# Kernel optimization log

Hardware: AMD Instinct MI355X
Metric: run time of the kernel (lower is better)

Reference implementation:

```python
import jax, jax.numpy as jnp
import numpy as np

B, L, A, D = 4, 512, 8, 256
H = 256  # hidden_dim
O = 256  # output_dim


def setup_inputs() -> dict:
    key = jax.random.key(0)
    ks = jax.random.split(key, 12)
    s = 0.05
    return {
        "x": jax.random.normal(ks[0], (B, L, A, D), dtype=jnp.float32),
        "conv_w": jax.random.normal(ks[1], (H, D), dtype=jnp.float32) * s,
        "conv_b": jax.random.normal(ks[2], (H,), dtype=jnp.float32) * s,
        "theta_w": jax.random.normal(ks[3], (H, H), dtype=jnp.float32) * s,
        "theta_b": jax.random.normal(ks[4], (H,), dtype=jnp.float32) * s,
        "phi_w": jax.random.normal(ks[5], (H, H), dtype=jnp.float32) * s,
        "phi_b": jax.random.normal(ks[6], (H,), dtype=jnp.float32) * s,
        "g_w": jax.random.normal(ks[7], (H, H), dtype=jnp.float32) * s,
        "g_b": jax.random.normal(ks[8], (H,), dtype=jnp.float32) * s,
        "f_w": jax.random.normal(ks[9], (O, H), dtype=jnp.float32) * s,
        "f_b": jax.random.normal(ks[10], (O,), dtype=jnp.float32) * s,
    }


def reference(x, conv_w, conv_b, theta_w, theta_b, phi_w, phi_b, g_w, g_b, f_w, f_b):
    batch, length, n_agents, _ = x.shape
    # residual: identity (input_dim == output_dim, stride 1)
    res = x
    # conv with kernel (1,1): pointwise projection over channel dim
    h = jnp.einsum('blad,hd->blah', x, conv_w) + conv_b  # [B,L,A,H]
    N = length * n_agents
    h = h.reshape(batch, N, H)
    theta = jnp.einsum('bnh,kh->bnk', h, theta_w) + theta_b  # [B,N,H]
    phi = jnp.einsum('bnh,kh->bnk', h, phi_w) + phi_b        # [B,N,H]
    g = jnp.einsum('bnh,kh->bnk', h, g_w) + g_b              # [B,N,H]
    scores = jnp.einsum('bnk,bmk->bnm', theta, phi) / jnp.sqrt(jnp.asarray(H, theta.dtype))
    y = jax.nn.softmax(scores, axis=2)                       # [B,N,N]
    z = jnp.einsum('bnm,bmk->bnk', y, g) / jnp.sqrt(jnp.asarray(N, y.dtype))
    out = jnp.einsum('bnk,ok->bno', z, f_w) + f_b            # [B,N,O]
    out = out.reshape(batch, length, n_agents, O)
    return out + res
```

## Files before the change

kernel.cpp:

```cpp
#include <hip/hip_runtime.h>

typedef unsigned short u16;
typedef __bf16 bf16x8 __attribute__((ext_vector_type(8)));
typedef float f32x4 __attribute__((ext_vector_type(4)));
typedef float f32x16 __attribute__((ext_vector_type(16)));
typedef float float4v __attribute__((ext_vector_type(4)));
typedef unsigned short u16x8 __attribute__((ext_vector_type(8)));
typedef unsigned short u16x4 __attribute__((ext_vector_type(4)));

#define MFMA16(a, b, c) __builtin_amdgcn_mfma_f32_16x16x32_bf16(a, b, c, 0, 0, 0)
#define MFMA32(a, b, c) __builtin_amdgcn_mfma_f32_32x32x16_bf16(a, b, c, 0, 0, 0)

__device__ __forceinline__ u16 f2bf(float f) {
  union { float f; unsigned u; } v; v.f = f;
  unsigned r = v.u + 0x7fffu + ((v.u >> 16) & 1u);
  return (u16)(r >> 16);
}
__device__ __forceinline__ float bf2f(u16 b) {
  union { unsigned u; float f; } v; v.u = ((unsigned)b) << 16;
  return v.f;
}

__device__ __forceinline__ void gload16(const void* g, void* l) {
  __builtin_amdgcn_global_load_lds(
      (__attribute__((address_space(1))) void*)g,
      (__attribute__((address_space(3))) void*)l, 16, 0, 0);
}

__device__ __forceinline__ unsigned cvtpk(float lo, float hi) {
  unsigned r;
  asm("v_cvt_pk_bf16_f32 %0, %1, %2" : "=v"(r) : "v"(lo), "v"(hi));
  return r;
}
__device__ __forceinline__ void plswap(unsigned& a, unsigned& b) {
  asm volatile("v_permlane32_swap_b32 %0, %1" : "+v"(a), "+v"(b));
}

__global__ __launch_bounds__(256) void convert_w(
    const float* __restrict__ cw,
    const float* __restrict__ tw, const float* __restrict__ pw,
    const float* __restrict__ gw, const float* __restrict__ fw,
    const float* __restrict__ tb, const float* __restrict__ pb,
    const float* __restrict__ gb,
    u16* __restrict__ cwb, u16* __restrict__ wcat, u16* __restrict__ fwb,
    float* __restrict__ bcat) {
  const int idx = blockIdx.x * 256 + threadIdx.x;
  const float* src;
  u16* dst;
  int off;
  if (idx < 16384)      { src = cw; dst = cwb;  off = idx; }
  else if (idx < 32768) { src = tw; dst = wcat; off = idx - 16384; }
  else if (idx < 49152) { src = pw; dst = wcat + 65536;  off = idx - 32768; }
  else if (idx < 65536) { src = gw; dst = wcat + 131072; off = idx - 49152; }
  else if (idx < 81920) { src = fw; dst = fwb;  off = idx - 65536; }
  else if (idx < 82112) {
    int j = (idx - 81920) * 4;
#pragma unroll
    for (int i = 0; i < 4; ++i) {
      int k = j + i;
      bcat[k] = (k < 256) ? tb[k] : (k < 512) ? pb[k - 256] : gb[k - 512];
    }
    return;
  } else return;
  float4v v = *(const float4v*)(src + (size_t)off * 4);
  u16x4 o;
#pragma unroll
  for (int i = 0; i < 4; ++i) o[i] = f2bf(v[i]);
  *(u16x4*)(dst + (size_t)off * 4) = o;
}

__global__ __launch_bounds__(256) void gemm_bt(
    const u16* __restrict__ A, const u16* __restrict__ W,
    const float* __restrict__ bias, u16* __restrict__ Cout, int K, int ldc) {
  __shared__ u16 As[8192];
  __shared__ u16 Bs[8192];
  const int t = threadIdx.x;
  const int lane = t & 63, w = t >> 6;
  const int brow = blockIdx.x * 128, bcol = blockIdx.y * 128;
  const int wr = (w >> 1) * 64, wc = (w & 1) * 64;
  f32x4 acc[4][4];
#pragma unroll
  for (int i = 0; i < 4; ++i)
#pragma unroll
    for (int j = 0; j < 4; ++j)
#pragma unroll
      for (int r = 0; r < 4; ++r) acc[i][j][r] = 0.0f;

  const int sr = t >> 3, sc8 = (t & 7) * 8;
  const u16* gA = A + (size_t)(brow + sr) * K + sc8;
  const u16* gW = W + (size_t)(bcol + sr) * K + sc8;

  for (int kt = 0; kt < K; kt += 64) {
#pragma unroll
    for (int c = 0; c < 4; ++c) {
      gload16(gA + (size_t)c * 32 * K + kt, &As[c * 2048 + t * 8]);
      gload16(gW + (size_t)c * 32 * K + kt, &Bs[c * 2048 + t * 8]);
    }
    __syncthreads();
#pragma unroll
    for (int kk = 0; kk < 2; ++kk) {
      const int ko = kk * 32 + (lane >> 4) * 8;
      bf16x8 af[4], bfr[4];
#pragma unroll
      for (int i = 0; i < 4; ++i)
        af[i] = *(const bf16x8*)(&As[(wr + i * 16 + (lane & 15)) * 64 + ko]);
#pragma unroll
      for (int j = 0; j < 4; ++j)
        bfr[j] = *(const bf16x8*)(&Bs[(wc + j * 16 + (lane & 15)) * 64 + ko]);
#pragma unroll
      for (int i = 0; i < 4; ++i)
#pragma unroll
        for (int j = 0; j < 4; ++j)
          acc[i][j] = MFMA16(af[i], bfr[j], acc[i][j]);
    }
    __syncthreads();
  }

  const int r0 = (lane >> 4) * 4, c0 = lane & 15;
#pragma unroll
  for (int i = 0; i < 4; ++i)
#pragma unroll
    for (int j = 0; j < 4; ++j) {
      const int col = bcol + wc + j * 16 + c0;
      const float bv = bias[col];
#pragma unroll
      for (int r = 0; r < 4; ++r) {
        const size_t o = (size_t)(brow + wr + i * 16 + r0 + r) * ldc + col;
        Cout[o] = f2bf(acc[i][j][r] + bv);
      }
    }
}

__global__ __launch_bounds__(256) void gemm_h(
    const float* __restrict__ X, const u16* __restrict__ W,
    const float* __restrict__ bias, u16* __restrict__ Cout) {
  __shared__ u16 As[8192];
  __shared__ u16 Bs[8192];
  const int t = threadIdx.x;
  const int lane = t & 63, w = t >> 6;
  const int brow = blockIdx.x * 128, bcol = blockIdx.y * 128;
  const int wr = (w >> 1) * 64, wc = (w & 1) * 64;
  f32x4 acc[4][4];
#pragma unroll
  for (int i = 0; i < 4; ++i)
#pragma unroll
    for (int j = 0; j < 4; ++j)
#pragma unroll
      for (int r = 0; r < 4; ++r) acc[i][j][r] = 0.0f;

  const int sr = t >> 3, sc8 = (t & 7) * 8;
  const u16* gW = W + (size_t)(bcol + sr) * 256 + sc8;
  const int ar = t & 127, ach = t >> 7;
  const float* gX = X + (size_t)(brow + ar) * 256 + ach * 32;

  for (int kt = 0; kt < 256; kt += 64) {
#pragma unroll
    for (int c = 0; c < 4; ++c)
      gload16(gW + (size_t)c * 32 * 256 + kt, &Bs[c * 2048 + t * 8]);
    u16x8 pk[4];
#pragma unroll
    for (int j = 0; j < 4; ++j) {
      float4v v0 = *(const float4v*)(gX + kt + j * 8);
      float4v v1 = *(const float4v*)(gX + kt + j * 8 + 4);
#pragma unroll
      for (int e = 0; e < 4; ++e) { pk[j][e] = f2bf(v0[e]); pk[j][4 + e] = f2bf(v1[e]); }
    }
#pragma unroll
    for (int j = 0; j < 4; ++j) {
      int unit = (ach * 4 + j) ^ (ar & 7);
      *(u16x8*)(&As[ar * 64 + unit * 8]) = pk[j];
    }
    __syncthreads();
#pragma unroll
    for (int kk = 0; kk < 2; ++kk) {
      const int ko = kk * 32 + (lane >> 4) * 8;
      bf16x8 af[4], bfr[4];
#pragma unroll
      for (int i = 0; i < 4; ++i) {
        int R = wr + i * 16 + (lane & 15);
        int unit = (kk * 4 + (lane >> 4)) ^ (R & 7);
        af[i] = *(const bf16x8*)(&As[R * 64 + unit * 8]);
      }
#pragma unroll
      for (int j = 0; j < 4; ++j)
        bfr[j] = *(const bf16x8*)(&Bs[(wc + j * 16 + (lane & 15)) * 64 + ko]);
#pragma unroll
      for (int i = 0; i < 4; ++i)
#pragma unroll
        for (int j = 0; j < 4; ++j)
          acc[i][j] = MFMA16(af[i], bfr[j], acc[i][j]);
    }
    __syncthreads();
  }

  const int r0 = (lane >> 4) * 4, c0 = lane & 15;
#pragma unroll
  for (int i = 0; i < 4; ++i)
#pragma unroll
    for (int j = 0; j < 4; ++j) {
      const int col = bcol + wc + j * 16 + c0;
      const float bv = bias[col];
#pragma unroll
      for (int r = 0; r < 4; ++r) {
        const size_t o = (size_t)(brow + wr + i * 16 + r0 + r) * 256 + col;
        Cout[o] = f2bf(acc[i][j][r] + bv);
      }
    }
}

__global__ __launch_bounds__(256) void transpose_g_k(
    const u16* __restrict__ tpg, u16* __restrict__ gT) {
  __shared__ u16 T[64][65];
  const int t = threadIdx.x;
  const int bm = (blockIdx.x & 63) * 64;
  const int bk = ((blockIdx.x >> 6) & 3) * 64;
  const int b = blockIdx.x >> 8;
  const int r = t >> 3, c8 = (t & 7) * 8;
#pragma unroll
  for (int ch = 0; ch < 2; ++ch) {
    u16x8 v = *(const u16x8*)(tpg + (size_t)(b * 4096 + bm + r + ch * 32) * 768 + 512 + bk + c8);
#pragma unroll
    for (int j = 0; j < 8; ++j) T[r + ch * 32][c8 + j] = v[j];
  }
  __syncthreads();
#pragma unroll
  for (int ch = 0; ch < 2; ++ch) {
    u16x8 o;
#pragma unroll
    for (int j = 0; j < 8; ++j) o[j] = T[c8 + j][r + ch * 32];
    *(u16x8*)(gT + (size_t)(b * 256 + bk + r + ch * 32) * 4096 + bm + c8) = o;
  }
}

__global__ __launch_bounds__(256, 2) void flash2(
    const u16* __restrict__ tpg, const u16* __restrict__ gT,
    u16* __restrict__ Zp, u16* __restrict__ Lpb) {
  __shared__ u16 Kl[2][32 * 256];
  __shared__ u16 Vl[2][256 * 32];

  const int t = threadIdx.x;
  const int lane = t & 63, w = t >> 6;
  const int l31 = lane & 31, hi = lane >> 5;
  const int bid = blockIdx.x;
  const int b = bid >> 7;
  const int quarter = (bid >> 5) & 3;
  const int qt = bid & 31;
  const int q0 = qt * 128 + w * 32;
  const int kv0 = quarter * 1024;

  bf16x8 q[16];
  {
    const u16* qp = tpg + (size_t)(b * 4096 + q0 + l31) * 768 + hi * 8;
#pragma unroll
    for (int ks = 0; ks < 16; ++ks) q[ks] = *(const bf16x8*)(qp + ks * 16);
  }

  f32x16 zacc[8];
#pragma unroll
  for (int i = 0; i < 8; ++i)
#pragma unroll
    for (int j = 0; j < 16; ++j) zacc[i][j] = 0.0f;
  float ell = 0.0f;

  const int ksr = t >> 5, ksc = t & 31;

  auto stage = [&](int tile, int bi) {
    const size_t krow0 = (size_t)(b * 4096 + kv0 + tile * 32);
#pragma unroll
    for (int ch = 0; ch < 4; ++ch) {
      int r = ch * 8 + ksr;
      gload16(tpg + (krow0 + r) * 768 + 256 + ((ksc ^ r) * 8), &Kl[bi][ch * 2048 + t * 8]);
    }
#pragma unroll
    for (int ch = 0; ch < 4; ++ch) {
      int u = ch * 256 + t;
      int r = u >> 2, c16 = u & 3;
      gload16(gT + (size_t)(b * 256 + r) * 4096 + kv0 + tile * 32 + ((c16 ^ ((r >> 1) & 3)) * 8),
              &Vl[bi][u * 8]);
    }
  };

  stage(0, 0);
  __syncthreads();

  for (int tile = 0; tile < 32; ++tile) {
    const int cur = tile & 1;
    if (tile + 1 < 32) stage(tile + 1, cur ^ 1);

    f32x16 s;
#pragma unroll
    for (int j = 0; j < 16; ++j) s[j] = 0.0f;
    const u16* kb = &Kl[cur][0];
    __builtin_amdgcn_s_setprio(1);
#pragma unroll
    for (int ks = 0; ks < 16; ++ks) {
      bf16x8 kf = *(const bf16x8*)(kb + l31 * 256 + (((2 * ks + hi) ^ l31) * 8));
      s = MFMA32(kf, q[ks], s);
    }
    __builtin_amdgcn_s_setprio(0);

    bf16x8 pa[2];
#pragma unroll
    for (int half = 0; half < 2; ++half) {
      float p[8];
#pragma unroll
      for (int g = 0; g < 8; ++g) {
        p[g] = __builtin_amdgcn_exp2f(s[half * 8 + g] * 0.09016844f);
        ell += p[g];
      }
      unsigned x0 = cvtpk(p[0], p[1]), y0 = cvtpk(p[4], p[5]);
      unsigned x1 = cvtpk(p[2], p[3]), y1 = cvtpk(p[6], p[7]);
      plswap(x0, y0);
      plswap(x1, y1);
      union { unsigned u[4]; bf16x8 v; } cc;
      cc.u[0] = x0; cc.u[1] = x1; cc.u[2] = y0; cc.u[3] = y1;
      pa[half] = cc.v;
    }

    const u16* vb = &Vl[cur][0];
    __builtin_amdgcn_s_setprio(1);
#pragma unroll
    for (int ks2 = 0; ks2 < 2; ++ks2) {
#pragma unroll
      for (int nt = 0; nt < 8; ++nt) {
        int row = nt * 32 + l31;
        bf16x8 vv = *(const bf16x8*)(vb + row * 32 + (((2 * ks2 + hi) ^ ((row >> 1) & 3)) * 8));
        zacc[nt] = MFMA32(pa[ks2], vv, zacc[nt]);
      }
    }
    __builtin_amdgcn_s_setprio(0);
    __syncthreads();
  }

  ell += __shfl_xor(ell, 32, 64);

#pragma unroll
  for (int g = 0; g < 16; ++g) {
    int r = (g & 3) + 8 * (g >> 2) + 4 * hi;
    size_t rowoff = ((size_t)(quarter * 16384 + b * 4096 + q0 + r)) * 256 + l31;
#pragma unroll
    for (int nt = 0; nt < 8; ++nt) Zp[rowoff + nt * 32] = f2bf(zacc[nt][g]);
  }
  if (lane < 32) Lpb[quarter * 16384 + b * 4096 + q0 + l31] = f2bf(ell);
}

__global__ __launch_bounds__(256) void gemm_out(
    const u16* __restrict__ Zp, const u16* __restrict__ Lpb,
    const u16* __restrict__ W, const float* __restrict__ bias,
    float* __restrict__ Cout, const float* __restrict__ res) {
  __shared__ u16 As[8192];
  __shared__ u16 Bs[8192];
  const int t = threadIdx.x;
  const int lane = t & 63, w = t >> 6;
  const int brow = blockIdx.x * 128, bcol = blockIdx.y * 128;
  const int wr = (w >> 1) * 64, wc = (w & 1) * 64;
  f32x4 acc[4][4];
#pragma unroll
  for (int i = 0; i < 4; ++i)
#pragma unroll
    for (int j = 0; j < 4; ++j)
#pragma unroll
      for (int r = 0; r < 4; ++r) acc[i][j][r] = 0.0f;

  const int sr = t >> 3, sc8 = (t & 7) * 8;
  const u16* gW = W + (size_t)(bcol + sr) * 256 + sc8;
  const int ar = t >> 1, ach = t & 1;
  const int am = brow + ar;
  const float linv = 1.0f /
      ((bf2f(Lpb[am]) + bf2f(Lpb[16384 + am]) + bf2f(Lpb[32768 + am]) + bf2f(Lpb[49152 + am])) *
       64.0f);

  for (int kt = 0; kt < 256; kt += 64) {
#pragma unroll
    for (int c = 0; c < 4; ++c)
      gload16(gW + (size_t)c * 32 * 256 + kt, &Bs[c * 2048 + t * 8]);
    const int col0 = kt + ach * 32;
    float sacc[32];
#pragma unroll
    for (int e = 0; e < 32; ++e) sacc[e] = 0.0f;
#pragma unroll
    for (int qd = 0; qd < 4; ++qd) {
      const u16* zp = Zp + ((size_t)(qd * 16384) + am) * 256 + col0;
#pragma unroll
      for (int j = 0; j < 4; ++j) {
        u16x8 v = *(const u16x8*)(zp + j * 8);
#pragma unroll
        for (int e = 0; e < 8; ++e) sacc[j * 8 + e] += bf2f(v[e]);
      }
    }
#pragma unroll
    for (int j = 0; j < 4; ++j) {
      u16x8 pk;
#pragma unroll
      for (int e = 0; e < 8; ++e) pk[e] = f2bf(sacc[j * 8 + e] * linv);
      int unit = (ach * 4 + j) ^ (ar & 7);
      *(u16x8*)(&As[ar * 64 + unit * 8]) = pk;
    }
    __syncthreads();
#pragma unroll
    for (int kk = 0; kk < 2; ++kk) {
      const int ko = kk * 32 + (lane >> 4) * 8;
      bf16x8 af[4], bfr[4];
#pragma unroll
      for (int i = 0; i < 4; ++i) {
        int R = wr + i * 16 + (lane & 15);
        int unit = (kk * 4 + (lane >> 4)) ^ (R & 7);
        af[i] = *(const bf16x8*)(&As[R * 64 + unit * 8]);
      }
#pragma unroll
      for (int j = 0; j < 4; ++j)
        bfr[j] = *(const bf16x8*)(&Bs[(wc + j * 16 + (lane & 15)) * 64 + ko]);
#pragma unroll
      for (int i = 0; i < 4; ++i)
#pragma unroll
        for (int j = 0; j < 4; ++j)
          acc[i][j] = MFMA16(af[i], bfr[j], acc[i][j]);
    }
    __syncthreads();
  }

  const int r0 = (lane >> 4) * 4, c0 = lane & 15;
#pragma unroll
  for (int i = 0; i < 4; ++i)
#pragma unroll
    for (int j = 0; j < 4; ++j) {
      const int col = bcol + wc + j * 16 + c0;
      const float bv = bias[col];
#pragma unroll
      for (int r = 0; r < 4; ++r) {
        const size_t o = (size_t)(brow + wr + i * 16 + r0 + r) * 256 + col;
        Cout[o] = acc[i][j][r] + bv + res[o];
      }
    }
}

extern "C" void kernel_launch(void* const* d_in, const int* in_sizes, int n_in,
                              void* d_out, int out_size, void* d_ws, size_t ws_size,
                              hipStream_t stream) {
  const float* x  = (const float*)d_in[0];
  const float* cw = (const float*)d_in[1];
  const float* cb = (const float*)d_in[2];
  const float* tw = (const float*)d_in[3];
  const float* tb = (const float*)d_in[4];
  const float* pw = (const float*)d_in[5];
  const float* pb = (const float*)d_in[6];
  const float* gw = (const float*)d_in[7];
  const float* gb = (const float*)d_in[8];
  const float* fw = (const float*)d_in[9];
  const float* fb = (const float*)d_in[10];

  char* ws = (char*)d_ws;
  u16*   tpg  = (u16*)(ws);
  u16*   gT   = (u16*)(ws + 25165824);
  u16*   hb   = (u16*)(ws + 41943040);
  u16*   Zp   = (u16*)(ws + 33554432);
  u16*   Lpb  = (u16*)(ws + 67108864);
  u16*   cwb  = (u16*)(ws + 67239936);
  u16*   wcat = (u16*)(ws + 67371008);
  u16*   fwb  = (u16*)(ws + 67764224);
  float* bcat = (float*)(ws + 67895296);

  convert_w<<<321, 256, 0, stream>>>(cw, tw, pw, gw, fw, tb, pb, gb,
                                     cwb, wcat, fwb, bcat);
  gemm_h<<<dim3(128, 2), 256, 0, stream>>>(x, cwb, cb, hb);
  gemm_bt<<<dim3(128, 6), 256, 0, stream>>>(hb, wcat, bcat, tpg, 256, 768);
  transpose_g_k<<<1024, 256, 0, stream>>>(tpg, gT);
  flash2<<<512, 256, 0, stream>>>(tpg, gT, Zp, Lpb);
  gemm_out<<<dim3(128, 2), 256, 0, stream>>>(Zp, Lpb, fwb, fb, (float*)d_out, x);
}
```

Baseline: 215.9 us.

## Fold conv projection into theta/phi/g weights and split QK accumulator chains

Precomputes fused weights W3·conv_w and fused biases in a prep kernel, so theta/phi/g are computed directly from x in one GEMM. This removes the separate h GEMM, its bf16 intermediate write and read, and the weight-conversion kernel. In flash2, the QK^T MFMA chain is split into two independent accumulators to shorten the dependency chain. The prep kernel does a small fp32 matmul per launch, and folding the weights changes where bf16 rounding happens.

```diff
diff --git a/kernel.cpp b/kernel.cpp
--- a/kernel.cpp
+++ b/kernel.cpp
@@ -36,102 +36,46 @@
   asm volatile("v_permlane32_swap_b32 %0, %1" : "+v"(a), "+v"(b));
 }
 
-__global__ __launch_bounds__(256) void convert_w(
-    const float* __restrict__ cw,
-    const float* __restrict__ tw, const float* __restrict__ pw,
-    const float* __restrict__ gw, const float* __restrict__ fw,
-    const float* __restrict__ tb, const float* __restrict__ pb,
-    const float* __restrict__ gb,
-    u16* __restrict__ cwb, u16* __restrict__ wcat, u16* __restrict__ fwb,
-    float* __restrict__ bcat) {
-  const int idx = blockIdx.x * 256 + threadIdx.x;
-  const float* src;
-  u16* dst;
-  int off;
-  if (idx < 16384)      { src = cw; dst = cwb;  off = idx; }
-  else if (idx < 32768) { src = tw; dst = wcat; off = idx - 16384; }
-  else if (idx < 49152) { src = pw; dst = wcat + 65536;  off = idx - 32768; }
-  else if (idx < 65536) { src = gw; dst = wcat + 131072; off = idx - 49152; }
-  else if (idx < 81920) { src = fw; dst = fwb;  off = idx - 65536; }
-  else if (idx < 82112) {
-    int j = (idx - 81920) * 4;
-#pragma unroll
-    for (int i = 0; i < 4; ++i) {
-      int k = j + i;
-      bcat[k] = (k < 256) ? tb[k] : (k < 512) ? pb[k - 256] : gb[k - 512];
-    }
+__global__ __launch_bounds__(256) void prep_k(
+    const float* __restrict__ cw, const float* __restrict__ tw,
+    const float* __restrict__ pw, const float* __restrict__ gw,
+    const float* __restrict__ cb, const float* __restrict__ tb,
+    const float* __restrict__ pb, const float* __restrict__ gb,
+    const float* __restrict__ fw,
+    u16* __restrict__ Wf, float* __restrict__ biasp, u16* __restrict__ fwb) {
+  const int t = threadIdx.x;
+  const int bid = blockIdx.x;
+  if (bid >= 768) {
+    const int idx = (bid - 768) * 256 + t;
+    float4v v = *(const float4v*)(fw + (size_t)idx * 4);
+    u16x4 o;
+#pragma unroll
+    for (int i = 0; i < 4; ++i) o[i] = f2bf(v[i]);
+    *(u16x4*)(fwb + (size_t)idx * 4) = o;
     return;
-  } else return;
-  float4v v = *(const float4v*)(src + (size_t)off * 4);
-  u16x4 o;
-#pragma unroll
-  for (int i = 0; i < 4; ++i) o[i] = f2bf(v[i]);
-  *(u16x4*)(dst + (size_t)off * 4) = o;
-}
-
-__global__ __launch_bounds__(256) void gemm_bt(
-    const u16* __restrict__ A, const u16* __restrict__ W,
-    const float* __restrict__ bias, u16* __restrict__ Cout, int K, int ldc) {
-  __shared__ u16 As[8192];
-  __shared__ u16 Bs[8192];
-  const int t = threadIdx.x;
-  const int lane = t & 63, w = t >> 6;
-  const int brow = blockIdx.x * 128, bcol = blockIdx.y * 128;
-  const int wr = (w >> 1) * 64, wc = (w & 1) * 64;
-  f32x4 acc[4][4];
-#pragma unroll
-  for (int i = 0; i < 4; ++i)
-#pragma unroll
-    for (int j = 0; j < 4; ++j)
-#pragma unroll
-      for (int r = 0; r < 4; ++r) acc[i][j][r] = 0.0f;
-
-  const int sr = t >> 3, sc8 = (t & 7) * 8;
-  const u16* gA = A + (size_t)(brow + sr) * K + sc8;
-  const u16* gW = W + (size_t)(bcol + sr) * K + sc8;
-
-  for (int kt = 0; kt < K; kt += 64) {
-#pragma unroll
-    for (int c = 0; c < 4; ++c) {
-      gload16(gA + (size_t)c * 32 * K + kt, &As[c * 2048 + t * 8]);
-      gload16(gW + (size_t)c * 32 * K + kt, &Bs[c * 2048 + t * 8]);
-    }
-    __syncthreads();
-#pragma unroll
-    for (int kk = 0; kk < 2; ++kk) {
-      const int ko = kk * 32 + (lane >> 4) * 8;
-      bf16x8 af[4], bfr[4];
-#pragma unroll
-      for (int i = 0; i < 4; ++i)
-        af[i] = *(const bf16x8*)(&As[(wr + i * 16 + (lane & 15)) * 64 + ko]);
-#pragma unroll
-      for (int j = 0; j < 4; ++j)
-        bfr[j] = *(const bf16x8*)(&Bs[(wc + j * 16 + (lane & 15)) * 64 + ko]);
-#pragma unroll
-      for (int i = 0; i < 4; ++i)
-#pragma unroll
-        for (int j = 0; j < 4; ++j)
-          acc[i][j] = MFMA16(af[i], bfr[j], acc[i][j]);
-    }
-    __syncthreads();
-  }
-
-  const int r0 = (lane >> 4) * 4, c0 = lane & 15;
-#pragma unroll
-  for (int i = 0; i < 4; ++i)
-#pragma unroll
-    for (int j = 0; j < 4; ++j) {
-      const int col = bcol + wc + j * 16 + c0;
-      const float bv = bias[col];
-#pragma unroll
-      for (int r = 0; r < 4; ++r) {
-        const size_t o = (size_t)(brow + wr + i * 16 + r0 + r) * ldc + col;
-        Cout[o] = f2bf(acc[i][j][r] + bv);
-      }
-    }
-}
-
-__global__ __launch_bounds__(256) void gemm_h(
+  }
+  const int n3 = bid;
+  const float* w3 = n3 < 256 ? tw + (size_t)n3 * 256
+                  : n3 < 512 ? pw + (size_t)(n3 - 256) * 256
+                             : gw + (size_t)(n3 - 512) * 256;
+  const float b3 = n3 < 256 ? tb[n3] : n3 < 512 ? pb[n3 - 256] : gb[n3 - 512];
+  __shared__ float w3s[256];
+  w3s[t] = w3[t];
+  __syncthreads();
+  float acc = 0.0f;
+#pragma unroll 8
+  for (int h = 0; h < 256; ++h) acc = fmaf(w3s[h], cw[(size_t)h * 256 + t], acc);
+  Wf[(size_t)n3 * 256 + t] = f2bf(acc);
+  float pv = w3s[t] * cb[t];
+#pragma unroll
+  for (int m = 1; m < 64; m <<= 1) pv += __shfl_xor(pv, m, 64);
+  __shared__ float red[4];
+  if ((t & 63) == 0) red[t >> 6] = pv;
+  __syncthreads();
+  if (t == 0) biasp[n3] = red[0] + red[1] + red[2] + red[3] + b3;
+}
+
+__global__ __launch_bounds__(256) void gemm_tpg(
     const float* __restrict__ X, const u16* __restrict__ W,
     const float* __restrict__ bias, u16* __restrict__ Cout) {
   __shared__ u16 As[8192];
@@ -202,7 +146,7 @@
       const float bv = bias[col];
 #pragma unroll
       for (int r = 0; r < 4; ++r) {
-        const size_t o = (size_t)(brow + wr + i * 16 + r0 + r) * 256 + col;
+        const size_t o = (size_t)(brow + wr + i * 16 + r0 + r) * 768 + col;
         Cout[o] = f2bf(acc[i][j][r] + bv);
       }
     }
@@ -287,17 +231,21 @@
     const int cur = tile & 1;
     if (tile + 1 < 32) stage(tile + 1, cur ^ 1);
 
-    f32x16 s;
-#pragma unroll
-    for (int j = 0; j < 16; ++j) s[j] = 0.0f;
+    f32x16 s0, s1;
+#pragma unroll
+    for (int j = 0; j < 16; ++j) { s0[j] = 0.0f; s1[j] = 0.0f; }
     const u16* kb = &Kl[cur][0];
     __builtin_amdgcn_s_setprio(1);
 #pragma unroll
-    for (int ks = 0; ks < 16; ++ks) {
-      bf16x8 kf = *(const bf16x8*)(kb + l31 * 256 + (((2 * ks + hi) ^ l31) * 8));
-      s = MFMA32(kf, q[ks], s);
+    for (int ks = 0; ks < 8; ++ks) {
+      bf16x8 kfa = *(const bf16x8*)(kb + l31 * 256 + (((2 * ks + hi) ^ l31) * 8));
+      bf16x8 kfb = *(const bf16x8*)(kb + l31 * 256 + (((2 * (ks + 8) + hi) ^ l31) * 8));
+      s0 = MFMA32(kfa, q[ks], s0);
+      s1 = MFMA32(kfb, q[ks + 8], s1);
     }
     __builtin_amdgcn_s_setprio(0);
+#pragma unroll
+    for (int j = 0; j < 16; ++j) s0[j] += s1[j];
 
     bf16x8 pa[2];
 #pragma unroll
@@ -305,7 +253,7 @@
       float p[8];
 #pragma unroll
       for (int g = 0; g < 8; ++g) {
-        p[g] = __builtin_amdgcn_exp2f(s[half * 8 + g] * 0.09016844f);
+        p[g] = __builtin_amdgcn_exp2f(s0[half * 8 + g] * 0.09016844f);
         ell += p[g];
       }
       unsigned x0 = cvtpk(p[0], p[1]), y0 = cvtpk(p[4], p[5]);
@@ -450,20 +398,16 @@
   const float* fb = (const float*)d_in[10];
 
   char* ws = (char*)d_ws;
-  u16*   tpg  = (u16*)(ws);
-  u16*   gT   = (u16*)(ws + 25165824);
-  u16*   hb   = (u16*)(ws + 41943040);
-  u16*   Zp   = (u16*)(ws + 33554432);
-  u16*   Lpb  = (u16*)(ws + 67108864);
-  u16*   cwb  = (u16*)(ws + 67239936);
-  u16*   wcat = (u16*)(ws + 67371008);
-  u16*   fwb  = (u16*)(ws + 67764224);
-  float* bcat = (float*)(ws + 67895296);
-
-  convert_w<<<321, 256, 0, stream>>>(cw, tw, pw, gw, fw, tb, pb, gb,
-                                     cwb, wcat, fwb, bcat);
-  gemm_h<<<dim3(128, 2), 256, 0, stream>>>(x, cwb, cb, hb);
-  gemm_bt<<<dim3(128, 6), 256, 0, stream>>>(hb, wcat, bcat, tpg, 256, 768);
+  u16*   tpg   = (u16*)(ws);
+  u16*   gT    = (u16*)(ws + 25165824);
+  u16*   Zp    = (u16*)(ws + 33554432);
+  u16*   Lpb   = (u16*)(ws + 67108864);
+  u16*   Wf    = (u16*)(ws + 67239936);
+  u16*   fwb   = (u16*)(ws + 67633152);
+  float* biasp = (float*)(ws + 67764224);
+
+  prep_k<<<832, 256, 0, stream>>>(cw, tw, pw, gw, cb, tb, pb, gb, fw, Wf, biasp, fwb);
+  gemm_tpg<<<dim3(128, 6), 256, 0, stream>>>(x, Wf, biasp, tpg);
   transpose_g_k<<<1024, 256, 0, stream>>>(tpg, gT);
   flash2<<<512, 256, 0, stream>>>(tpg, gT, Zp, Lpb);
   gemm_out<<<dim3(128, 2), 256, 0, stream>>>(Zp, Lpb, fwb, fb, (float*)d_out, x);
```

Measured after the change: 244.1 us. +13.1%, slower.
